# Optimization experiments

Hardware: AMD Instinct MI355X
Metric: run time of the kernel (lower is better)

Reference implementation:

```python
import jax, jax.numpy as jnp
import numpy as np

FINAL_OUT = 28
NPG = 127            # nodes per graph (XENON1T top PMT array)
B = 4096             # graphs per batch
N = B * NPG          # 520192 total nodes
EPG = 2032           # edges per graph (avg degree ~16)
E = B * EPG          # 8323072 total edges


def setup_inputs() -> dict:
    key = jax.random.key(0)
    ks = jax.random.split(key, 12)
    # intra-graph random edges, offset per graph
    off = (jnp.arange(B, dtype=jnp.int64) * NPG)[:, None]
    src = (jax.random.randint(ks[0], (B, EPG), 0, NPG) + off).reshape(-1)
    dst = (jax.random.randint(ks[1], (B, EPG), 0, NPG) + off).reshape(-1)
    edge_index = jnp.stack([src, dst]).astype(jnp.int64)
    x = jax.random.normal(ks[2], (N, 3), dtype=jnp.float32)
    # GCNConv weights (in,out) + bias; Linear head weights (in,out) + bias
    def glorot(k, shape):
        lim = float(np.sqrt(6.0 / (shape[0] + shape[1])))
        return jax.random.uniform(k, shape, jnp.float32, -lim, lim)
    return {
        "x": x,
        "edge_index": edge_index,
        "W1": glorot(ks[3], (3, 16)),
        "b1": jnp.zeros((16,), jnp.float32),
        "W2": glorot(ks[4], (16, FINAL_OUT)),
        "b2": jnp.zeros((FINAL_OUT,), jnp.float32),
        "lw1": glorot(ks[5], (FINAL_OUT * NPG, 16)),
        "lb1": jnp.zeros((16,), jnp.float32),
        "lw2": glorot(ks[6], (16, 2)),
        "lb2": jnp.zeros((2,), jnp.float32),
    }


def _gcn_conv(x, W, b, src_sl, dst_sl, dinv):
    # h = X W, then normalized scatter-add aggregation over edges (+self-loops)
    h = x @ W                                   # [N, F_out]
    norm = dinv[src_sl] * dinv[dst_sl]          # [E+N]
    msg = h[src_sl] * norm[:, None]             # gather + scale
    return jax.ops.segment_sum(msg, dst_sl, num_segments=N) + b


def reference(x, edge_index, W1, b1, W2, b2, lw1, lb1, lw2, lb2):
    src, dst = edge_index[0], edge_index[1]
    loops = jnp.arange(N, dtype=edge_index.dtype)
    src_sl = jnp.concatenate([src, loops])
    dst_sl = jnp.concatenate([dst, loops])
    # symmetric degree normalization with self-loops (PyG GCNConv default)
    deg = jnp.zeros((N,), jnp.float32).at[dst_sl].add(1.0)
    dinv = jnp.where(deg > 0, jax.lax.rsqrt(deg), 0.0)
    h = jax.nn.relu(_gcn_conv(x, W1, b1, src_sl, dst_sl, dinv))
    h = jax.nn.relu(_gcn_conv(h, W2, b2, src_sl, dst_sl, dinv))
    g = h.reshape(-1, FINAL_OUT * NPG)          # [B, 3556]
    g = jax.nn.relu(g @ lw1 + lb1)
    return g @ lw2 + lb2                        # [B, 2]
```

## Files before the change

### kernel.cpp

```cpp
#include <hip/hip_runtime.h>

#define NPG 127
#define EPG 2032
#define NGRAPH 4096
#define NE (EPG * NGRAPH)
#define F1 16
#define F2 28

#define EPK  0
#define A2   0
#define XS   2032
#define HS2  2540
#define H2   4572
#define XRAW 4572
#define ARENA 8128

__global__ __launch_bounds__(256, 4) void gcn_fused(
    const float* __restrict__ x, const int* __restrict__ ei,
    const float* __restrict__ W1, const float* __restrict__ b1,
    const float* __restrict__ W2, const float* __restrict__ b2,
    const float* __restrict__ lw1, const float* __restrict__ lb1,
    const float* __restrict__ lw2, const float* __restrict__ lb2,
    float* __restrict__ out)
{
    __shared__ __align__(16) float arena[ARENA];
    __shared__ unsigned short csr[EPG];
    __shared__ int starts[NPG + 1];
    __shared__ int cursor[NPG];
    __shared__ float dinv[NPG];
    __shared__ float w1s[48], b1s[F1], w2s[F1 * F2], b2s[F2];
    __shared__ float lb1s[16], lw2s[32], lb2s[2];
    __shared__ float wsum[64];
    __shared__ float gsh[16];
    __shared__ int is64;

    const int t = threadIdx.x;
    const int g = blockIdx.x;
    const int nodebase = g * NPG;
    const int ebase = g * EPG;

    if (t < 64) {
        int w = ei[2 * t + 1];
        unsigned long long m = __ballot(w != 0);
        if (t == 0) is64 = (m == 0ULL) ? 1 : 0;
    }
    if (t < NPG + 1) starts[t] = 0;
    if (t < 48)       w1s[t]        = W1[t];
    else if (t < 64)  b1s[t - 48]   = b1[t - 48];
    else if (t < 92)  b2s[t - 64]   = b2[t - 64];
    else if (t < 108) lb1s[t - 92]  = lb1[t - 92];
    else if (t < 140) lw2s[t - 108] = lw2[t - 108];
    else if (t < 142) lb2s[t - 140] = lb2[t - 140];
    for (int i = t; i < F1 * F2; i += 256) w2s[i] = W2[i];
    __syncthreads();

    int* epk = (int*)&arena[EPK];
    if (is64) {
        const long long* ei64 = (const long long*)ei;
        const longlong2* s2 = (const longlong2*)(ei64 + ebase);
        const longlong2* d2 = (const longlong2*)(ei64 + NE + ebase);
        for (int q = t; q < EPG / 2; q += 256) {
            longlong2 ss = s2[q], dd = d2[q];
            int s0 = (int)ss.x - nodebase, d0 = (int)dd.x - nodebase;
            int s1 = (int)ss.y - nodebase, d1 = (int)dd.y - nodebase;
            epk[2 * q + 0] = (s0 << 8) | d0;  atomicAdd(&starts[d0 + 1], 1);
            epk[2 * q + 1] = (s1 << 8) | d1;  atomicAdd(&starts[d1 + 1], 1);
        }
    } else {
        const int4* s4 = (const int4*)(ei + ebase);
        const int4* d4 = (const int4*)(ei + NE + ebase);
        for (int q = t; q < EPG / 4; q += 256) {
            int4 ss = s4[q], dd = d4[q];
            int e0 = 4 * q;
            epk[e0 + 0] = ((ss.x - nodebase) << 8) | (dd.x - nodebase);
            epk[e0 + 1] = ((ss.y - nodebase) << 8) | (dd.y - nodebase);
            epk[e0 + 2] = ((ss.z - nodebase) << 8) | (dd.z - nodebase);
            epk[e0 + 3] = ((ss.w - nodebase) << 8) | (dd.w - nodebase);
            atomicAdd(&starts[(dd.x - nodebase) + 1], 1);
            atomicAdd(&starts[(dd.y - nodebase) + 1], 1);
            atomicAdd(&starts[(dd.z - nodebase) + 1], 1);
            atomicAdd(&starts[(dd.w - nodebase) + 1], 1);
        }
    }
    for (int i = t; i < NPG * 3; i += 256) arena[XRAW + i] = x[nodebase * 3 + i];
    __syncthreads();
    if (t < NPG) dinv[t] = rsqrtf((float)(starts[t + 1] + 1));
    __syncthreads();
    #pragma unroll
    for (int off = 1; off < 128; off <<= 1) {
        int v = 0;
        if (t < 128) { v = starts[t]; if (t >= off) v += starts[t - off]; }
        __syncthreads();
        if (t < 128) starts[t] = v;
        __syncthreads();
    }
    if (t < NPG) {
        cursor[t] = starts[t];
        float di = dinv[t];
        float4 xr;
        xr.x = arena[XRAW + t * 3 + 0] * di;
        xr.y = arena[XRAW + t * 3 + 1] * di;
        xr.z = arena[XRAW + t * 3 + 2] * di;
        xr.w = 0.f;
        *(float4*)&arena[XS + t * 4] = xr;
    }
    __syncthreads();
    for (int e = t; e < EPG; e += 256) {
        int pk = epk[e];
        int d = pk & 255, s = pk >> 8;
        int pos = atomicAdd(&cursor[d], 1);
        csr[pos] = (unsigned short)s;
    }
    __syncthreads();

    if (t < 2 * NPG) {
        const int i = t >> 1, half = t & 1;
        const int e0 = starts[i], e1 = starts[i + 1];
        float ax = 0.f, ay = 0.f, az = 0.f;
        for (int k = e0 + half; k < e1; k += 2) {
            int s = csr[k];
            const float4 v = *(const float4*)&arena[XS + s * 4];
            ax += v.x; ay += v.y; az += v.z;
        }
        if (!half) {
            const float4 v = *(const float4*)&arena[XS + i * 4];
            ax += v.x; ay += v.y; az += v.z;
        }
        ax += __shfl_xor(ax, 1);
        ay += __shfl_xor(ay, 1);
        az += __shfl_xor(az, 1);
        const float di = dinv[i];
        ax *= di; ay *= di; az *= di;
        const int fb = half * 8;
        float h[8];
        #pragma unroll
        for (int f = 0; f < 8; ++f) {
            float v = ax * w1s[fb + f] + ay * w1s[16 + fb + f] + az * w1s[32 + fb + f];
            h[f] = fmaxf(v + b1s[fb + f], 0.f) * di;
        }
        const int rot = (i >> 1) & 3;
        const int s0 = ((half * 2 + 0) + rot) & 3;
        const int s1 = ((half * 2 + 1) + rot) & 3;
        *(float4*)&arena[HS2 + i * 16 + s0 * 4] = make_float4(h[0], h[1], h[2], h[3]);
        *(float4*)&arena[HS2 + i * 16 + s1 * 4] = make_float4(h[4], h[5], h[6], h[7]);
    }
    __syncthreads();

    if (t < 2 * NPG) {
        const int i = t >> 1, half = t & 1;
        const int e0 = starts[i], e1 = starts[i + 1];
        float4 c0 = {0,0,0,0}, c1 = {0,0,0,0}, c2 = {0,0,0,0}, c3 = {0,0,0,0};
        for (int k = e0 + half; k < e1; k += 2) {
            int s = csr[k];
            const int b = HS2 + s * 16;
            const int r = (s >> 1) & 3;
            const float4 v0 = *(const float4*)&arena[b + (((0 + r) & 3) << 2)];
            const float4 v1 = *(const float4*)&arena[b + (((1 + r) & 3) << 2)];
            const float4 v2 = *(const float4*)&arena[b + (((2 + r) & 3) << 2)];
            const float4 v3 = *(const float4*)&arena[b + (((3 + r) & 3) << 2)];
            c0.x += v0.x; c0.y += v0.y; c0.z += v0.z; c0.w += v0.w;
            c1.x += v1.x; c1.y += v1.y; c1.z += v1.z; c1.w += v1.w;
            c2.x += v2.x; c2.y += v2.y; c2.z += v2.z; c2.w += v2.w;
            c3.x += v3.x; c3.y += v3.y; c3.z += v3.z; c3.w += v3.w;
        }
        if (!half) {
            const int b = HS2 + i * 16;
            const int r = (i >> 1) & 3;
            const float4 v0 = *(const float4*)&arena[b + (((0 + r) & 3) << 2)];
            const float4 v1 = *(const float4*)&arena[b + (((1 + r) & 3) << 2)];
            const float4 v2 = *(const float4*)&arena[b + (((2 + r) & 3) << 2)];
            const float4 v3 = *(const float4*)&arena[b + (((3 + r) & 3) << 2)];
            c0.x += v0.x; c0.y += v0.y; c0.z += v0.z; c0.w += v0.w;
            c1.x += v1.x; c1.y += v1.y; c1.z += v1.z; c1.w += v1.w;
            c2.x += v2.x; c2.y += v2.y; c2.z += v2.z; c2.w += v2.w;
            c3.x += v3.x; c3.y += v3.y; c3.z += v3.z; c3.w += v3.w;
        }
        c0.x += __shfl_xor(c0.x, 1); c0.y += __shfl_xor(c0.y, 1);
        c0.z += __shfl_xor(c0.z, 1); c0.w += __shfl_xor(c0.w, 1);
        c1.x += __shfl_xor(c1.x, 1); c1.y += __shfl_xor(c1.y, 1);
        c1.z += __shfl_xor(c1.z, 1); c1.w += __shfl_xor(c1.w, 1);
        c2.x += __shfl_xor(c2.x, 1); c2.y += __shfl_xor(c2.y, 1);
        c2.z += __shfl_xor(c2.z, 1); c2.w += __shfl_xor(c2.w, 1);
        c3.x += __shfl_xor(c3.x, 1); c3.y += __shfl_xor(c3.y, 1);
        c3.z += __shfl_xor(c3.z, 1); c3.w += __shfl_xor(c3.w, 1);
        const float di = dinv[i];
        if (!half) {
            c0.x *= di; c0.y *= di; c0.z *= di; c0.w *= di;
            c1.x *= di; c1.y *= di; c1.z *= di; c1.w *= di;
            *(float4*)&arena[A2 + i * 16 + 0] = c0;
            *(float4*)&arena[A2 + i * 16 + 4] = c1;
        } else {
            c2.x *= di; c2.y *= di; c2.z *= di; c2.w *= di;
            c3.x *= di; c3.y *= di; c3.z *= di; c3.w *= di;
            *(float4*)&arena[A2 + i * 16 + 8]  = c2;
            *(float4*)&arena[A2 + i * 16 + 12] = c3;
        }
    }
    __syncthreads();

    if (t < 252) {
        const int f2 = t % 28, ic = t / 28;
        float wc[16];
        #pragma unroll
        for (int k = 0; k < 16; ++k) wc[k] = w2s[k * F2 + f2];
        const float bb = b2s[f2];
        for (int i = ic; i < NPG; i += 9) {
            const float4 h0 = *(const float4*)&arena[A2 + i * 16 + 0];
            const float4 h1v = *(const float4*)&arena[A2 + i * 16 + 4];
            const float4 h2v = *(const float4*)&arena[A2 + i * 16 + 8];
            const float4 h3 = *(const float4*)&arena[A2 + i * 16 + 12];
            float acc = bb;
            acc = fmaf(h0.x, wc[0], acc);  acc = fmaf(h0.y, wc[1], acc);
            acc = fmaf(h0.z, wc[2], acc);  acc = fmaf(h0.w, wc[3], acc);
            acc = fmaf(h1v.x, wc[4], acc); acc = fmaf(h1v.y, wc[5], acc);
            acc = fmaf(h1v.z, wc[6], acc); acc = fmaf(h1v.w, wc[7], acc);
            acc = fmaf(h2v.x, wc[8], acc); acc = fmaf(h2v.y, wc[9], acc);
            acc = fmaf(h2v.z, wc[10], acc); acc = fmaf(h2v.w, wc[11], acc);
            acc = fmaf(h3.x, wc[12], acc); acc = fmaf(h3.y, wc[13], acc);
            acc = fmaf(h3.z, wc[14], acc); acc = fmaf(h3.w, wc[15], acc);
            arena[H2 + i * F2 + f2] = fmaxf(acc, 0.f);
        }
    }
    __syncthreads();

    float pj[16];
    #pragma unroll
    for (int j = 0; j < 16; ++j) pj[j] = 0.f;
    const float4* lw14 = (const float4*)lw1;
    for (int r = t; r < NPG * F2; r += 256) {
        float hv = arena[H2 + r];
        float4 a = lw14[r * 4 + 0];
        float4 b = lw14[r * 4 + 1];
        float4 c = lw14[r * 4 + 2];
        float4 d = lw14[r * 4 + 3];
        pj[0]  = fmaf(hv, a.x, pj[0]);  pj[1]  = fmaf(hv, a.y, pj[1]);
        pj[2]  = fmaf(hv, a.z, pj[2]);  pj[3]  = fmaf(hv, a.w, pj[3]);
        pj[4]  = fmaf(hv, b.x, pj[4]);  pj[5]  = fmaf(hv, b.y, pj[5]);
        pj[6]  = fmaf(hv, b.z, pj[6]);  pj[7]  = fmaf(hv, b.w, pj[7]);
        pj[8]  = fmaf(hv, c.x, pj[8]);  pj[9]  = fmaf(hv, c.y, pj[9]);
        pj[10] = fmaf(hv, c.z, pj[10]); pj[11] = fmaf(hv, c.w, pj[11]);
        pj[12] = fmaf(hv, d.x, pj[12]); pj[13] = fmaf(hv, d.y, pj[13]);
        pj[14] = fmaf(hv, d.z, pj[14]); pj[15] = fmaf(hv, d.w, pj[15]);
    }
    #pragma unroll
    for (int j = 0; j < 16; ++j) {
        float v = pj[j];
        v += __shfl_xor(v, 1);
        v += __shfl_xor(v, 2);
        v += __shfl_xor(v, 4);
        v += __shfl_xor(v, 8);
        v += __shfl_xor(v, 16);
        v += __shfl_xor(v, 32);
        pj[j] = v;
    }
    if ((t & 63) == 0) {
        int wid = t >> 6;
        #pragma unroll
        for (int j = 0; j < 16; ++j) wsum[wid * 16 + j] = pj[j];
    }
    __syncthreads();
    if (t < 16) {
        float s = wsum[t] + wsum[16 + t] + wsum[32 + t] + wsum[48 + t];
        gsh[t] = fmaxf(s + lb1s[t], 0.f);
    }
    __syncthreads();
    if (t < 2) {
        float o = lb2s[t];
        #pragma unroll
        for (int j = 0; j < 16; ++j) o = fmaf(gsh[j], lw2s[j * 2 + t], o);
        out[g * 2 + t] = o;
    }
}

extern "C" void kernel_launch(void* const* d_in, const int* in_sizes, int n_in,
                              void* d_out, int out_size, void* d_ws, size_t ws_size,
                              hipStream_t stream) {
    const float* x   = (const float*)d_in[0];
    const int*   ei  = (const int*)d_in[1];
    const float* W1  = (const float*)d_in[2];
    const float* b1  = (const float*)d_in[3];
    const float* W2  = (const float*)d_in[4];
    const float* b2  = (const float*)d_in[5];
    const float* lw1 = (const float*)d_in[6];
    const float* lb1 = (const float*)d_in[7];
    const float* lw2 = (const float*)d_in[8];
    const float* lb2 = (const float*)d_in[9];
    float* out = (float*)d_out;

    gcn_fused<<<NGRAPH, 256, 0, stream>>>(x, ei, W1, b1, W2, b2,
                                          lw1, lb1, lw2, lb2, out);
}
```

Baseline: 194.6 us.

## Process one graph per wavefront with wave-local CSR build and no block barriers

Restructures the fused GCN kernel so each 64-lane wavefront handles a whole graph, with four graphs per block. Block-wide __syncthreads are replaced by lgkmcnt waits. The prefix sum becomes a shuffle scan, and the CSR is built directly with byte indices in a per-wave LDS region. The second-layer transform now runs per node in registers, and the final head reduction happens inside the wave. The aim is to remove barrier and idle-thread costs. In exchange, each lane now serially aggregates two nodes, which raises per-lane work and register pressure (launch bounds drop to 2 blocks per SM). It also relies on wave-synchronous LDS visibility.

```diff
diff --git a/kernel.cpp b/kernel.cpp
--- a/kernel.cpp
+++ b/kernel.cpp
@@ -4,18 +4,112 @@
 #define EPG 2032
 #define NGRAPH 4096
 #define NE (EPG * NGRAPH)
-#define F1 16
-#define F2 28
-
-#define EPK  0
-#define A2   0
-#define XS   2032
-#define HS2  2540
-#define H2   4572
-#define XRAW 4572
-#define ARENA 8128
-
-__global__ __launch_bounds__(256, 4) void gcn_fused(
+
+#define WREG 3812
+#define R_CSR    0
+#define R_STARTS 508
+#define R_CURSOR 636
+#define R_XS     764
+#define R_HS2    1272
+#define R_H2     0
+
+#define WFENCE() asm volatile("s_waitcnt lgkmcnt(0)" ::: "memory")
+
+__device__ __forceinline__ void agg1_node(float* A, const unsigned* st,
+        const unsigned char* csr8, int i, float di,
+        float sx, float sy, float sz, const float* w1s, const float* b1s)
+{
+    float ax = sx, ay = sy, az = sz;
+    const unsigned e0 = st[i], e1 = st[i + 1];
+    for (unsigned k = e0; k < e1; ++k) {
+        const int s = csr8[k];
+        const float4 v = *(const float4*)(A + R_XS + s * 4);
+        ax += v.x; ay += v.y; az += v.z;
+    }
+    ax *= di; ay *= di; az *= di;
+    float* hrow = A + R_HS2 + i * 20;
+    #pragma unroll
+    for (int f4 = 0; f4 < 4; ++f4) {
+        const float4 wa = *(const float4*)(w1s + f4 * 4);
+        const float4 wb = *(const float4*)(w1s + 16 + f4 * 4);
+        const float4 wc = *(const float4*)(w1s + 32 + f4 * 4);
+        const float4 bb = *(const float4*)(b1s + f4 * 4);
+        float4 h;
+        h.x = fmaxf(fmaf(ax, wa.x, fmaf(ay, wb.x, fmaf(az, wc.x, bb.x))), 0.f) * di;
+        h.y = fmaxf(fmaf(ax, wa.y, fmaf(ay, wb.y, fmaf(az, wc.y, bb.y))), 0.f) * di;
+        h.z = fmaxf(fmaf(ax, wa.z, fmaf(ay, wb.z, fmaf(az, wc.z, bb.z))), 0.f) * di;
+        h.w = fmaxf(fmaf(ax, wa.w, fmaf(ay, wb.w, fmaf(az, wc.w, bb.w))), 0.f) * di;
+        *(float4*)(hrow + f4 * 4) = h;
+    }
+}
+
+__device__ __forceinline__ void agg2_node(const float* A, const unsigned* st,
+        const unsigned char* csr8, int i, float di,
+        float4& c0, float4& c1, float4& c2, float4& c3)
+{
+    const float* base = A + R_HS2;
+    const float* r = base + i * 20;
+    c0 = *(const float4*)(r);
+    c1 = *(const float4*)(r + 4);
+    c2 = *(const float4*)(r + 8);
+    c3 = *(const float4*)(r + 12);
+    const unsigned e0 = st[i], e1 = st[i + 1];
+    for (unsigned k = e0; k < e1; ++k) {
+        const int s = csr8[k];
+        const float* p = base + s * 20;
+        const float4 v0 = *(const float4*)(p);
+        const float4 v1 = *(const float4*)(p + 4);
+        const float4 v2 = *(const float4*)(p + 8);
+        const float4 v3 = *(const float4*)(p + 12);
+        c0.x += v0.x; c0.y += v0.y; c0.z += v0.z; c0.w += v0.w;
+        c1.x += v1.x; c1.y += v1.y; c1.z += v1.z; c1.w += v1.w;
+        c2.x += v2.x; c2.y += v2.y; c2.z += v2.z; c2.w += v2.w;
+        c3.x += v3.x; c3.y += v3.y; c3.z += v3.z; c3.w += v3.w;
+    }
+    c0.x *= di; c0.y *= di; c0.z *= di; c0.w *= di;
+    c1.x *= di; c1.y *= di; c1.z *= di; c1.w *= di;
+    c2.x *= di; c2.y *= di; c2.z *= di; c2.w *= di;
+    c3.x *= di; c3.y *= di; c3.z *= di; c3.w *= di;
+}
+
+__device__ __forceinline__ void transform_node(float* A, int i,
+        float4 c0, float4 c1, float4 c2, float4 c3,
+        const float* w2s, const float* b2s)
+{
+    float acc[28];
+    #pragma unroll
+    for (int f4 = 0; f4 < 7; ++f4) {
+        const float4 b = *(const float4*)(b2s + f4 * 4);
+        acc[f4 * 4 + 0] = b.x; acc[f4 * 4 + 1] = b.y;
+        acc[f4 * 4 + 2] = b.z; acc[f4 * 4 + 3] = b.w;
+    }
+    const float a2arr[16] = {c0.x, c0.y, c0.z, c0.w, c1.x, c1.y, c1.z, c1.w,
+                             c2.x, c2.y, c2.z, c2.w, c3.x, c3.y, c3.z, c3.w};
+    #pragma unroll
+    for (int k = 0; k < 16; ++k) {
+        const float a = a2arr[k];
+        #pragma unroll
+        for (int f4 = 0; f4 < 7; ++f4) {
+            const float4 wv = *(const float4*)(w2s + k * 28 + f4 * 4);
+            acc[f4 * 4 + 0] = fmaf(a, wv.x, acc[f4 * 4 + 0]);
+            acc[f4 * 4 + 1] = fmaf(a, wv.y, acc[f4 * 4 + 1]);
+            acc[f4 * 4 + 2] = fmaf(a, wv.z, acc[f4 * 4 + 2]);
+            acc[f4 * 4 + 3] = fmaf(a, wv.w, acc[f4 * 4 + 3]);
+        }
+    }
+    float* hrow = A + R_H2 + i * 28;
+    #pragma unroll
+    for (int f4 = 0; f4 < 7; ++f4) {
+        float4 h;
+        h.x = fmaxf(acc[f4 * 4 + 0], 0.f);
+        h.y = fmaxf(acc[f4 * 4 + 1], 0.f);
+        h.z = fmaxf(acc[f4 * 4 + 2], 0.f);
+        h.w = fmaxf(acc[f4 * 4 + 3], 0.f);
+        *(float4*)(hrow + f4 * 4) = h;
+    }
+}
+
+__global__ __launch_bounds__(256, 2) void gcn_fused(
     const float* __restrict__ x, const int* __restrict__ ei,
     const float* __restrict__ W1, const float* __restrict__ b1,
     const float* __restrict__ W2, const float* __restrict__ b2,
@@ -23,224 +117,152 @@
     const float* __restrict__ lw2, const float* __restrict__ lb2,
     float* __restrict__ out)
 {
-    __shared__ __align__(16) float arena[ARENA];
-    __shared__ unsigned short csr[EPG];
-    __shared__ int starts[NPG + 1];
-    __shared__ int cursor[NPG];
-    __shared__ float dinv[NPG];
-    __shared__ float w1s[48], b1s[F1], w2s[F1 * F2], b2s[F2];
-    __shared__ float lb1s[16], lw2s[32], lb2s[2];
-    __shared__ float wsum[64];
-    __shared__ float gsh[16];
-    __shared__ int is64;
+    __shared__ __align__(16) float arena[4 * WREG];
+    __shared__ __align__(16) float w1s[48], b1s[16], w2s[448], b2s[28];
+    __shared__ __align__(16) float lb1s[16], lw2s[32], lb2s[2];
 
     const int t = threadIdx.x;
-    const int g = blockIdx.x;
-    const int nodebase = g * NPG;
-    const int ebase = g * EPG;
-
-    if (t < 64) {
-        int w = ei[2 * t + 1];
-        unsigned long long m = __ballot(w != 0);
-        if (t == 0) is64 = (m == 0ULL) ? 1 : 0;
-    }
-    if (t < NPG + 1) starts[t] = 0;
+    const int lane = t & 63;
+    const int w = t >> 6;
+    const int gi = blockIdx.x * 4 + w;
+    float* A = arena + w * WREG;
+    unsigned* cnt = (unsigned*)(A + R_STARTS);
+    unsigned* cur = (unsigned*)(A + R_CURSOR);
+    unsigned char* csr8 = (unsigned char*)(A + R_CSR);
+    const int nodebase = gi * NPG;
+    const long ebase = (long)gi * EPG;
+
     if (t < 48)       w1s[t]        = W1[t];
     else if (t < 64)  b1s[t - 48]   = b1[t - 48];
     else if (t < 92)  b2s[t - 64]   = b2[t - 64];
     else if (t < 108) lb1s[t - 92]  = lb1[t - 92];
     else if (t < 140) lw2s[t - 108] = lw2[t - 108];
     else if (t < 142) lb2s[t - 140] = lb2[t - 140];
-    for (int i = t; i < F1 * F2; i += 256) w2s[i] = W2[i];
+    for (int i = t; i < 448; i += 256) w2s[i] = W2[i];
+
+    const int hiw = ei[2 * lane + 1];
+    const bool is64 = (__ballot(hiw != 0) == 0ULL);
+
+    cnt[lane] = 0u;
+    cnt[lane + 64] = 0u;
+    WFENCE();
     __syncthreads();
 
-    int* epk = (int*)&arena[EPK];
+    if (is64) {
+        const long long* ei64 = (const long long*)ei;
+        const longlong2* d2 = (const longlong2*)(ei64 + NE + ebase);
+        for (int q = lane; q < EPG / 2; q += 64) {
+            const longlong2 dd = d2[q];
+            atomicAdd(&cnt[(int)dd.x - nodebase], 1u);
+            atomicAdd(&cnt[(int)dd.y - nodebase], 1u);
+        }
+    } else {
+        const int4* d4 = (const int4*)(ei + NE + ebase);
+        for (int q = lane; q < EPG / 4; q += 64) {
+            const int4 dd = d4[q];
+            atomicAdd(&cnt[dd.x - nodebase], 1u);
+            atomicAdd(&cnt[dd.y - nodebase], 1u);
+            atomicAdd(&cnt[dd.z - nodebase], 1u);
+            atomicAdd(&cnt[dd.w - nodebase], 1u);
+        }
+    }
+    WFENCE();
+
+    const int i0 = lane, i1 = lane + 64;
+    const bool v1 = (i1 < NPG);
+    const unsigned deg0 = cnt[i0];
+    const unsigned deg1 = v1 ? cnt[i1] : 0u;
+    const unsigned c0 = cnt[2 * lane], c1 = cnt[2 * lane + 1];
+    const float d0 = rsqrtf((float)(deg0 + 1u));
+    const float d1 = rsqrtf((float)(deg1 + 1u));
+    asm volatile("" ::: "memory");
+    unsigned ps = c0 + c1, sc = ps;
+    #pragma unroll
+    for (int dd = 1; dd < 64; dd <<= 1) {
+        const unsigned u = __shfl_up(sc, dd);
+        if (lane >= dd) sc += u;
+    }
+    const unsigned excl = sc - ps;
+    cnt[2 * lane] = excl;
+    cnt[2 * lane + 1] = excl + c0;
+    cur[2 * lane] = excl;
+    cur[2 * lane + 1] = excl + c0;
+
+    float sx0, sy0, sz0, sx1 = 0.f, sy1 = 0.f, sz1 = 0.f;
+    {
+        const float* xp = x + (long)(nodebase + i0) * 3;
+        sx0 = xp[0] * d0; sy0 = xp[1] * d0; sz0 = xp[2] * d0;
+        const float4 xv = {sx0, sy0, sz0, 0.f};
+        *(float4*)(A + R_XS + i0 * 4) = xv;
+        if (v1) {
+            const float* xq = x + (long)(nodebase + i1) * 3;
+            sx1 = xq[0] * d1; sy1 = xq[1] * d1; sz1 = xq[2] * d1;
+            const float4 xw = {sx1, sy1, sz1, 0.f};
+            *(float4*)(A + R_XS + i1 * 4) = xw;
+        }
+    }
+    WFENCE();
+
     if (is64) {
         const long long* ei64 = (const long long*)ei;
         const longlong2* s2 = (const longlong2*)(ei64 + ebase);
         const longlong2* d2 = (const longlong2*)(ei64 + NE + ebase);
-        for (int q = t; q < EPG / 2; q += 256) {
-            longlong2 ss = s2[q], dd = d2[q];
-            int s0 = (int)ss.x - nodebase, d0 = (int)dd.x - nodebase;
-            int s1 = (int)ss.y - nodebase, d1 = (int)dd.y - nodebase;
-            epk[2 * q + 0] = (s0 << 8) | d0;  atomicAdd(&starts[d0 + 1], 1);
-            epk[2 * q + 1] = (s1 << 8) | d1;  atomicAdd(&starts[d1 + 1], 1);
+        for (int q = lane; q < EPG / 2; q += 64) {
+            const longlong2 ss = s2[q], dd = d2[q];
+            unsigned p0 = atomicAdd(&cur[(int)dd.x - nodebase], 1u);
+            csr8[p0] = (unsigned char)((int)ss.x - nodebase);
+            unsigned p1 = atomicAdd(&cur[(int)dd.y - nodebase], 1u);
+            csr8[p1] = (unsigned char)((int)ss.y - nodebase);
         }
     } else {
         const int4* s4 = (const int4*)(ei + ebase);
         const int4* d4 = (const int4*)(ei + NE + ebase);
-        for (int q = t; q < EPG / 4; q += 256) {
-            int4 ss = s4[q], dd = d4[q];
-            int e0 = 4 * q;
-            epk[e0 + 0] = ((ss.x - nodebase) << 8) | (dd.x - nodebase);
-            epk[e0 + 1] = ((ss.y - nodebase) << 8) | (dd.y - nodebase);
-            epk[e0 + 2] = ((ss.z - nodebase) << 8) | (dd.z - nodebase);
-            epk[e0 + 3] = ((ss.w - nodebase) << 8) | (dd.w - nodebase);
-            atomicAdd(&starts[(dd.x - nodebase) + 1], 1);
-            atomicAdd(&starts[(dd.y - nodebase) + 1], 1);
-            atomicAdd(&starts[(dd.z - nodebase) + 1], 1);
-            atomicAdd(&starts[(dd.w - nodebase) + 1], 1);
-        }
-    }
-    for (int i = t; i < NPG * 3; i += 256) arena[XRAW + i] = x[nodebase * 3 + i];
-    __syncthreads();
-    if (t < NPG) dinv[t] = rsqrtf((float)(starts[t + 1] + 1));
-    __syncthreads();
-    #pragma unroll
-    for (int off = 1; off < 128; off <<= 1) {
-        int v = 0;
-        if (t < 128) { v = starts[t]; if (t >= off) v += starts[t - off]; }
-        __syncthreads();
-        if (t < 128) starts[t] = v;
-        __syncthreads();
-    }
-    if (t < NPG) {
-        cursor[t] = starts[t];
-        float di = dinv[t];
-        float4 xr;
-        xr.x = arena[XRAW + t * 3 + 0] * di;
-        xr.y = arena[XRAW + t * 3 + 1] * di;
-        xr.z = arena[XRAW + t * 3 + 2] * di;
-        xr.w = 0.f;
-        *(float4*)&arena[XS + t * 4] = xr;
-    }
-    __syncthreads();
-    for (int e = t; e < EPG; e += 256) {
-        int pk = epk[e];
-        int d = pk & 255, s = pk >> 8;
-        int pos = atomicAdd(&cursor[d], 1);
-        csr[pos] = (unsigned short)s;
-    }
-    __syncthreads();
-
-    if (t < 2 * NPG) {
-        const int i = t >> 1, half = t & 1;
-        const int e0 = starts[i], e1 = starts[i + 1];
-        float ax = 0.f, ay = 0.f, az = 0.f;
-        for (int k = e0 + half; k < e1; k += 2) {
-            int s = csr[k];
-            const float4 v = *(const float4*)&arena[XS + s * 4];
-            ax += v.x; ay += v.y; az += v.z;
-        }
-        if (!half) {
-            const float4 v = *(const float4*)&arena[XS + i * 4];
-            ax += v.x; ay += v.y; az += v.z;
-        }
-        ax += __shfl_xor(ax, 1);
-        ay += __shfl_xor(ay, 1);
-        az += __shfl_xor(az, 1);
-        const float di = dinv[i];
-        ax *= di; ay *= di; az *= di;
-        const int fb = half * 8;
-        float h[8];
-        #pragma unroll
-        for (int f = 0; f < 8; ++f) {
-            float v = ax * w1s[fb + f] + ay * w1s[16 + fb + f] + az * w1s[32 + fb + f];
-            h[f] = fmaxf(v + b1s[fb + f], 0.f) * di;
-        }
-        const int rot = (i >> 1) & 3;
-        const int s0 = ((half * 2 + 0) + rot) & 3;
-        const int s1 = ((half * 2 + 1) + rot) & 3;
-        *(float4*)&arena[HS2 + i * 16 + s0 * 4] = make_float4(h[0], h[1], h[2], h[3]);
-        *(float4*)&arena[HS2 + i * 16 + s1 * 4] = make_float4(h[4], h[5], h[6], h[7]);
-    }
-    __syncthreads();
-
-    if (t < 2 * NPG) {
-        const int i = t >> 1, half = t & 1;
-        const int e0 = starts[i], e1 = starts[i + 1];
-        float4 c0 = {0,0,0,0}, c1 = {0,0,0,0}, c2 = {0,0,0,0}, c3 = {0,0,0,0};
-        for (int k = e0 + half; k < e1; k += 2) {
-            int s = csr[k];
-            const int b = HS2 + s * 16;
-            const int r = (s >> 1) & 3;
-            const float4 v0 = *(const float4*)&arena[b + (((0 + r) & 3) << 2)];
-            const float4 v1 = *(const float4*)&arena[b + (((1 + r) & 3) << 2)];
-            const float4 v2 = *(const float4*)&arena[b + (((2 + r) & 3) << 2)];
-            const float4 v3 = *(const float4*)&arena[b + (((3 + r) & 3) << 2)];
-            c0.x += v0.x; c0.y += v0.y; c0.z += v0.z; c0.w += v0.w;
-            c1.x += v1.x; c1.y += v1.y; c1.z += v1.z; c1.w += v1.w;
-            c2.x += v2.x; c2.y += v2.y; c2.z += v2.z; c2.w += v2.w;
-            c3.x += v3.x; c3.y += v3.y; c3.z += v3.z; c3.w += v3.w;
-        }
-        if (!half) {
-            const int b = HS2 + i * 16;
-            const int r = (i >> 1) & 3;
-            const float4 v0 = *(const float4*)&arena[b + (((0 + r) & 3) << 2)];
-            const float4 v1 = *(const float4*)&arena[b + (((1 + r) & 3) << 2)];
-            const float4 v2 = *(const float4*)&arena[b + (((2 + r) & 3) << 2)];
-            const float4 v3 = *(const float4*)&arena[b + (((3 + r) & 3) << 2)];
-            c0.x += v0.x; c0.y += v0.y; c0.z += v0.z; c0.w += v0.w;
-            c1.x += v1.x; c1.y += v1.y; c1.z += v1.z; c1.w += v1.w;
-            c2.x += v2.x; c2.y += v2.y; c2.z += v2.z; c2.w += v2.w;
-            c3.x += v3.x; c3.y += v3.y; c3.z += v3.z; c3.w += v3.w;
-        }
-        c0.x += __shfl_xor(c0.x, 1); c0.y += __shfl_xor(c0.y, 1);
-        c0.z += __shfl_xor(c0.z, 1); c0.w += __shfl_xor(c0.w, 1);
-        c1.x += __shfl_xor(c1.x, 1); c1.y += __shfl_xor(c1.y, 1);
-        c1.z += __shfl_xor(c1.z, 1); c1.w += __shfl_xor(c1.w, 1);
-        c2.x += __shfl_xor(c2.x, 1); c2.y += __shfl_xor(c2.y, 1);
-        c2.z += __shfl_xor(c2.z, 1); c2.w += __shfl_xor(c2.w, 1);
-        c3.x += __shfl_xor(c3.x, 1); c3.y += __shfl_xor(c3.y, 1);
-        c3.z += __shfl_xor(c3.z, 1); c3.w += __shfl_xor(c3.w, 1);
-        const float di = dinv[i];
-        if (!half) {
-            c0.x *= di; c0.y *= di; c0.z *= di; c0.w *= di;
-            c1.x *= di; c1.y *= di; c1.z *= di; c1.w *= di;
-            *(float4*)&arena[A2 + i * 16 + 0] = c0;
-            *(float4*)&arena[A2 + i * 16 + 4] = c1;
-        } else {
-            c2.x *= di; c2.y *= di; c2.z *= di; c2.w *= di;
-            c3.x *= di; c3.y *= di; c3.z *= di; c3.w *= di;
-            *(float4*)&arena[A2 + i * 16 + 8]  = c2;
-            *(float4*)&arena[A2 + i * 16 + 12] = c3;
-        }
-    }
-    __syncthreads();
-
-    if (t < 252) {
-        const int f2 = t % 28, ic = t / 28;
-        float wc[16];
-        #pragma unroll
-        for (int k = 0; k < 16; ++k) wc[k] = w2s[k * F2 + f2];
-        const float bb = b2s[f2];
-        for (int i = ic; i < NPG; i += 9) {
-            const float4 h0 = *(const float4*)&arena[A2 + i * 16 + 0];
-            const float4 h1v = *(const float4*)&arena[A2 + i * 16 + 4];
-            const float4 h2v = *(const float4*)&arena[A2 + i * 16 + 8];
-            const float4 h3 = *(const float4*)&arena[A2 + i * 16 + 12];
-            float acc = bb;
-            acc = fmaf(h0.x, wc[0], acc);  acc = fmaf(h0.y, wc[1], acc);
-            acc = fmaf(h0.z, wc[2], acc);  acc = fmaf(h0.w, wc[3], acc);
-            acc = fmaf(h1v.x, wc[4], acc); acc = fmaf(h1v.y, wc[5], acc);
-            acc = fmaf(h1v.z, wc[6], acc); acc = fmaf(h1v.w, wc[7], acc);
-            acc = fmaf(h2v.x, wc[8], acc); acc = fmaf(h2v.y, wc[9], acc);
-            acc = fmaf(h2v.z, wc[10], acc); acc = fmaf(h2v.w, wc[11], acc);
-            acc = fmaf(h3.x, wc[12], acc); acc = fmaf(h3.y, wc[13], acc);
-            acc = fmaf(h3.z, wc[14], acc); acc = fmaf(h3.w, wc[15], acc);
-            arena[H2 + i * F2 + f2] = fmaxf(acc, 0.f);
-        }
-    }
-    __syncthreads();
+        for (int q = lane; q < EPG / 4; q += 64) {
+            const int4 ss = s4[q], dd = d4[q];
+            unsigned p0 = atomicAdd(&cur[dd.x - nodebase], 1u);
+            csr8[p0] = (unsigned char)(ss.x - nodebase);
+            unsigned p1 = atomicAdd(&cur[dd.y - nodebase], 1u);
+            csr8[p1] = (unsigned char)(ss.y - nodebase);
+            unsigned p2 = atomicAdd(&cur[dd.z - nodebase], 1u);
+            csr8[p2] = (unsigned char)(ss.z - nodebase);
+            unsigned p3 = atomicAdd(&cur[dd.w - nodebase], 1u);
+            csr8[p3] = (unsigned char)(ss.w - nodebase);
+        }
+    }
+    WFENCE();
+
+    const unsigned* st = cnt;
+    agg1_node(A, st, csr8, i0, d0, sx0, sy0, sz0, w1s, b1s);
+    if (v1) agg1_node(A, st, csr8, i1, d1, sx1, sy1, sz1, w1s, b1s);
+    WFENCE();
+
+    float4 a0, a1, a2, a3, e0v, e1v, e2v, e3v;
+    agg2_node(A, st, csr8, i0, d0, a0, a1, a2, a3);
+    if (v1) agg2_node(A, st, csr8, i1, d1, e0v, e1v, e2v, e3v);
+    WFENCE();
+
+    transform_node(A, i0, a0, a1, a2, a3, w2s, b2s);
+    if (v1) transform_node(A, i1, e0v, e1v, e2v, e3v, w2s, b2s);
+    WFENCE();
 
     float pj[16];
     #pragma unroll
     for (int j = 0; j < 16; ++j) pj[j] = 0.f;
     const float4* lw14 = (const float4*)lw1;
-    for (int r = t; r < NPG * F2; r += 256) {
-        float hv = arena[H2 + r];
-        float4 a = lw14[r * 4 + 0];
-        float4 b = lw14[r * 4 + 1];
-        float4 c = lw14[r * 4 + 2];
-        float4 d = lw14[r * 4 + 3];
-        pj[0]  = fmaf(hv, a.x, pj[0]);  pj[1]  = fmaf(hv, a.y, pj[1]);
-        pj[2]  = fmaf(hv, a.z, pj[2]);  pj[3]  = fmaf(hv, a.w, pj[3]);
-        pj[4]  = fmaf(hv, b.x, pj[4]);  pj[5]  = fmaf(hv, b.y, pj[5]);
-        pj[6]  = fmaf(hv, b.z, pj[6]);  pj[7]  = fmaf(hv, b.w, pj[7]);
-        pj[8]  = fmaf(hv, c.x, pj[8]);  pj[9]  = fmaf(hv, c.y, pj[9]);
-        pj[10] = fmaf(hv, c.z, pj[10]); pj[11] = fmaf(hv, c.w, pj[11]);
-        pj[12] = fmaf(hv, d.x, pj[12]); pj[13] = fmaf(hv, d.y, pj[13]);
-        pj[14] = fmaf(hv, d.z, pj[14]); pj[15] = fmaf(hv, d.w, pj[15]);
+    for (int r = lane; r < NPG * 28; r += 64) {
+        const float hv = A[R_H2 + r];
+        const float4 aa = lw14[(long)r * 4 + 0];
+        const float4 bb = lw14[(long)r * 4 + 1];
+        const float4 cc = lw14[(long)r * 4 + 2];
+        const float4 ddv = lw14[(long)r * 4 + 3];
+        pj[0]  = fmaf(hv, aa.x, pj[0]);  pj[1]  = fmaf(hv, aa.y, pj[1]);
+        pj[2]  = fmaf(hv, aa.z, pj[2]);  pj[3]  = fmaf(hv, aa.w, pj[3]);
+        pj[4]  = fmaf(hv, bb.x, pj[4]);  pj[5]  = fmaf(hv, bb.y, pj[5]);
+        pj[6]  = fmaf(hv, bb.z, pj[6]);  pj[7]  = fmaf(hv, bb.w, pj[7]);
+        pj[8]  = fmaf(hv, cc.x, pj[8]);  pj[9]  = fmaf(hv, cc.y, pj[9]);
+        pj[10] = fmaf(hv, cc.z, pj[10]); pj[11] = fmaf(hv, cc.w, pj[11]);
+        pj[12] = fmaf(hv, ddv.x, pj[12]); pj[13] = fmaf(hv, ddv.y, pj[13]);
+        pj[14] = fmaf(hv, ddv.z, pj[14]); pj[15] = fmaf(hv, ddv.w, pj[15]);
     }
     #pragma unroll
     for (int j = 0; j < 16; ++j) {
@@ -251,24 +273,13 @@
         v += __shfl_xor(v, 8);
         v += __shfl_xor(v, 16);
         v += __shfl_xor(v, 32);
-        pj[j] = v;
-    }
-    if ((t & 63) == 0) {
-        int wid = t >> 6;
+        pj[j] = fmaxf(v + lb1s[j], 0.f);
+    }
+    if (lane < 2) {
+        float o = lb2s[lane];
         #pragma unroll
-        for (int j = 0; j < 16; ++j) wsum[wid * 16 + j] = pj[j];
-    }
-    __syncthreads();
-    if (t < 16) {
-        float s = wsum[t] + wsum[16 + t] + wsum[32 + t] + wsum[48 + t];
-        gsh[t] = fmaxf(s + lb1s[t], 0.f);
-    }
-    __syncthreads();
-    if (t < 2) {
-        float o = lb2s[t];
-        #pragma unroll
-        for (int j = 0; j < 16; ++j) o = fmaf(gsh[j], lw2s[j * 2 + t], o);
-        out[g * 2 + t] = o;
+        for (int j = 0; j < 16; ++j) o = fmaf(pj[j], lw2s[j * 2 + lane], o);
+        out[gi * 2 + lane] = o;
     }
 }
 
@@ -287,6 +298,6 @@
     const float* lb2 = (const float*)d_in[9];
     float* out = (float*)d_out;
 
-    gcn_fused<<<NGRAPH, 256, 0, stream>>>(x, ei, W1, b1, W2, b2,
-                                          lw1, lb1, lw2, lb2, out);
-}
+    gcn_fused<<<NGRAPH / 4, 256, 0, stream>>>(x, ei, W1, b1, W2, b2,
+                                              lw1, lb1, lw2, lb2, out);
+}
```

Measured after the change: 282.8 us. 1.45x slower.

## Shrink LDS arena, use wave-shuffle scan, fuse layer-2 transform into registers

Applied to the files above, without the earlier changes.

Cuts the shared-memory footprint by overlapping buffers, storing CSR indices as bytes inside the arena, and reading x directly from global memory, then raises launch bounds from 4 to 6 blocks per CU. The multi-barrier Hillis-Steele prefix sum over starts is replaced with a single-wave shuffle scan over per-node counts. The layer-2 aggregation result stays in registers, and each thread pair computes 14 of the 28 output features directly, which removes an LDS round trip and a sync. The higher occupancy target may force register spills given the 14-element accumulators and 16-element arrays.

```diff
diff --git a/kernel.cpp b/kernel.cpp
--- a/kernel.cpp
+++ b/kernel.cpp
@@ -7,15 +7,14 @@
 #define F1 16
 #define F2 28
 
-#define EPK  0
-#define A2   0
-#define XS   2032
-#define HS2  2540
-#define H2   4572
-#define XRAW 4572
-#define ARENA 8128
-
-__global__ __launch_bounds__(256, 4) void gcn_fused(
+#define A_EPK 0
+#define A_HS2 0
+#define A_XS  2032
+#define A_CSR 2540
+#define A_H2  0
+#define ARENA 3556
+
+__global__ __launch_bounds__(256, 6) void gcn_fused(
     const float* __restrict__ x, const int* __restrict__ ei,
     const float* __restrict__ W1, const float* __restrict__ b1,
     const float* __restrict__ W2, const float* __restrict__ b2,
@@ -24,152 +23,152 @@
     float* __restrict__ out)
 {
     __shared__ __align__(16) float arena[ARENA];
-    __shared__ unsigned short csr[EPG];
-    __shared__ int starts[NPG + 1];
-    __shared__ int cursor[NPG];
+    __shared__ unsigned cnt[128], starts[128], cursor[128];
     __shared__ float dinv[NPG];
-    __shared__ float w1s[48], b1s[F1], w2s[F1 * F2], b2s[F2];
+    __shared__ __align__(16) float w1s[48], b1s[F1], w2s[448], b2s[F2];
     __shared__ float lb1s[16], lw2s[32], lb2s[2];
-    __shared__ float wsum[64];
-    __shared__ float gsh[16];
+    __shared__ float wsum[64], gsh[16];
     __shared__ int is64;
 
     const int t = threadIdx.x;
     const int g = blockIdx.x;
     const int nodebase = g * NPG;
-    const int ebase = g * EPG;
+    const long ebase = (long)g * EPG;
 
     if (t < 64) {
-        int w = ei[2 * t + 1];
-        unsigned long long m = __ballot(w != 0);
+        const int hiw = ei[2 * t + 1];
+        const unsigned long long m = __ballot(hiw != 0);
         if (t == 0) is64 = (m == 0ULL) ? 1 : 0;
     }
-    if (t < NPG + 1) starts[t] = 0;
     if (t < 48)       w1s[t]        = W1[t];
     else if (t < 64)  b1s[t - 48]   = b1[t - 48];
     else if (t < 92)  b2s[t - 64]   = b2[t - 64];
     else if (t < 108) lb1s[t - 92]  = lb1[t - 92];
     else if (t < 140) lw2s[t - 108] = lw2[t - 108];
     else if (t < 142) lb2s[t - 140] = lb2[t - 140];
-    for (int i = t; i < F1 * F2; i += 256) w2s[i] = W2[i];
-    __syncthreads();
-
-    int* epk = (int*)&arena[EPK];
+    for (int q = t; q < 448; q += 256) w2s[q] = W2[q];
+    if (t < 128) cnt[t] = 0u;
+    __syncthreads();
+
+    int* epk = (int*)&arena[A_EPK];
     if (is64) {
         const long long* ei64 = (const long long*)ei;
         const longlong2* s2 = (const longlong2*)(ei64 + ebase);
         const longlong2* d2 = (const longlong2*)(ei64 + NE + ebase);
         for (int q = t; q < EPG / 2; q += 256) {
-            longlong2 ss = s2[q], dd = d2[q];
-            int s0 = (int)ss.x - nodebase, d0 = (int)dd.x - nodebase;
-            int s1 = (int)ss.y - nodebase, d1 = (int)dd.y - nodebase;
-            epk[2 * q + 0] = (s0 << 8) | d0;  atomicAdd(&starts[d0 + 1], 1);
-            epk[2 * q + 1] = (s1 << 8) | d1;  atomicAdd(&starts[d1 + 1], 1);
+            const longlong2 ss = s2[q], dd = d2[q];
+            const int sa = (int)ss.x - nodebase, da = (int)dd.x - nodebase;
+            const int sb = (int)ss.y - nodebase, db = (int)dd.y - nodebase;
+            epk[2 * q + 0] = (sa << 8) | da;  atomicAdd(&cnt[da], 1u);
+            epk[2 * q + 1] = (sb << 8) | db;  atomicAdd(&cnt[db], 1u);
         }
     } else {
         const int4* s4 = (const int4*)(ei + ebase);
         const int4* d4 = (const int4*)(ei + NE + ebase);
         for (int q = t; q < EPG / 4; q += 256) {
-            int4 ss = s4[q], dd = d4[q];
-            int e0 = 4 * q;
-            epk[e0 + 0] = ((ss.x - nodebase) << 8) | (dd.x - nodebase);
-            epk[e0 + 1] = ((ss.y - nodebase) << 8) | (dd.y - nodebase);
-            epk[e0 + 2] = ((ss.z - nodebase) << 8) | (dd.z - nodebase);
-            epk[e0 + 3] = ((ss.w - nodebase) << 8) | (dd.w - nodebase);
-            atomicAdd(&starts[(dd.x - nodebase) + 1], 1);
-            atomicAdd(&starts[(dd.y - nodebase) + 1], 1);
-            atomicAdd(&starts[(dd.z - nodebase) + 1], 1);
-            atomicAdd(&starts[(dd.w - nodebase) + 1], 1);
-        }
-    }
-    for (int i = t; i < NPG * 3; i += 256) arena[XRAW + i] = x[nodebase * 3 + i];
-    __syncthreads();
-    if (t < NPG) dinv[t] = rsqrtf((float)(starts[t + 1] + 1));
-    __syncthreads();
-    #pragma unroll
-    for (int off = 1; off < 128; off <<= 1) {
-        int v = 0;
-        if (t < 128) { v = starts[t]; if (t >= off) v += starts[t - off]; }
-        __syncthreads();
-        if (t < 128) starts[t] = v;
-        __syncthreads();
+            const int4 ss = s4[q], dd = d4[q];
+            const int eb = 4 * q;
+            epk[eb + 0] = ((ss.x - nodebase) << 8) | (dd.x - nodebase);
+            epk[eb + 1] = ((ss.y - nodebase) << 8) | (dd.y - nodebase);
+            epk[eb + 2] = ((ss.z - nodebase) << 8) | (dd.z - nodebase);
+            epk[eb + 3] = ((ss.w - nodebase) << 8) | (dd.w - nodebase);
+            atomicAdd(&cnt[dd.x - nodebase], 1u);
+            atomicAdd(&cnt[dd.y - nodebase], 1u);
+            atomicAdd(&cnt[dd.z - nodebase], 1u);
+            atomicAdd(&cnt[dd.w - nodebase], 1u);
+        }
+    }
+    __syncthreads();
+
+    if (t < 64) {
+        const unsigned ca = cnt[2 * t], cb = cnt[2 * t + 1];
+        const unsigned ps = ca + cb;
+        unsigned sc = ps;
+        #pragma unroll
+        for (int d = 1; d < 64; d <<= 1) {
+            const unsigned u = __shfl_up(sc, d);
+            if (t >= d) sc += u;
+        }
+        const unsigned excl = sc - ps;
+        starts[2 * t] = excl;            cursor[2 * t] = excl;
+        starts[2 * t + 1] = excl + ca;   cursor[2 * t + 1] = excl + ca;
     }
     if (t < NPG) {
-        cursor[t] = starts[t];
-        float di = dinv[t];
-        float4 xr;
-        xr.x = arena[XRAW + t * 3 + 0] * di;
-        xr.y = arena[XRAW + t * 3 + 1] * di;
-        xr.z = arena[XRAW + t * 3 + 2] * di;
-        xr.w = 0.f;
-        *(float4*)&arena[XS + t * 4] = xr;
-    }
-    __syncthreads();
+        const float dv = rsqrtf((float)(cnt[t] + 1u));
+        dinv[t] = dv;
+        const float* xp = x + (long)(nodebase + t) * 3;
+        const float4 xv = {xp[0] * dv, xp[1] * dv, xp[2] * dv, 0.f};
+        *(float4*)&arena[A_XS + t * 4] = xv;
+    }
+    __syncthreads();
+
+    unsigned char* csr8 = (unsigned char*)&arena[A_CSR];
     for (int e = t; e < EPG; e += 256) {
-        int pk = epk[e];
-        int d = pk & 255, s = pk >> 8;
-        int pos = atomicAdd(&cursor[d], 1);
-        csr[pos] = (unsigned short)s;
-    }
-    __syncthreads();
-
-    if (t < 2 * NPG) {
-        const int i = t >> 1, half = t & 1;
-        const int e0 = starts[i], e1 = starts[i + 1];
+        const int pk = epk[e];
+        const int d = pk & 255, s = pk >> 8;
+        const unsigned pos = atomicAdd(&cursor[d], 1u);
+        csr8[pos] = (unsigned char)s;
+    }
+    __syncthreads();
+
+    const int i = t >> 1, half = t & 1;
+    const bool act = (t < 2 * NPG);
+    float di = 0.f; unsigned e0 = 0, e1 = 0;
+    if (act) { di = dinv[i]; e0 = starts[i]; e1 = starts[i + 1]; }
+
+    if (act) {
         float ax = 0.f, ay = 0.f, az = 0.f;
-        for (int k = e0 + half; k < e1; k += 2) {
-            int s = csr[k];
-            const float4 v = *(const float4*)&arena[XS + s * 4];
+        for (unsigned k = e0 + half; k < e1; k += 2) {
+            const int s = csr8[k];
+            const float4 v = *(const float4*)&arena[A_XS + s * 4];
             ax += v.x; ay += v.y; az += v.z;
         }
         if (!half) {
-            const float4 v = *(const float4*)&arena[XS + i * 4];
+            const float4 v = *(const float4*)&arena[A_XS + i * 4];
             ax += v.x; ay += v.y; az += v.z;
         }
         ax += __shfl_xor(ax, 1);
         ay += __shfl_xor(ay, 1);
         az += __shfl_xor(az, 1);
-        const float di = dinv[i];
         ax *= di; ay *= di; az *= di;
         const int fb = half * 8;
         float h[8];
         #pragma unroll
         for (int f = 0; f < 8; ++f) {
-            float v = ax * w1s[fb + f] + ay * w1s[16 + fb + f] + az * w1s[32 + fb + f];
+            const float v = ax * w1s[fb + f] + ay * w1s[16 + fb + f]
+                          + az * w1s[32 + fb + f];
             h[f] = fmaxf(v + b1s[fb + f], 0.f) * di;
         }
         const int rot = (i >> 1) & 3;
-        const int s0 = ((half * 2 + 0) + rot) & 3;
-        const int s1 = ((half * 2 + 1) + rot) & 3;
-        *(float4*)&arena[HS2 + i * 16 + s0 * 4] = make_float4(h[0], h[1], h[2], h[3]);
-        *(float4*)&arena[HS2 + i * 16 + s1 * 4] = make_float4(h[4], h[5], h[6], h[7]);
-    }
-    __syncthreads();
-
-    if (t < 2 * NPG) {
-        const int i = t >> 1, half = t & 1;
-        const int e0 = starts[i], e1 = starts[i + 1];
-        float4 c0 = {0,0,0,0}, c1 = {0,0,0,0}, c2 = {0,0,0,0}, c3 = {0,0,0,0};
-        for (int k = e0 + half; k < e1; k += 2) {
-            int s = csr[k];
-            const int b = HS2 + s * 16;
-            const int r = (s >> 1) & 3;
-            const float4 v0 = *(const float4*)&arena[b + (((0 + r) & 3) << 2)];
-            const float4 v1 = *(const float4*)&arena[b + (((1 + r) & 3) << 2)];
-            const float4 v2 = *(const float4*)&arena[b + (((2 + r) & 3) << 2)];
-            const float4 v3 = *(const float4*)&arena[b + (((3 + r) & 3) << 2)];
+        const int sl0 = (half * 2 + 0 + rot) & 3;
+        const int sl1 = (half * 2 + 1 + rot) & 3;
+        *(float4*)&arena[A_HS2 + i * 16 + sl0 * 4] = make_float4(h[0], h[1], h[2], h[3]);
+        *(float4*)&arena[A_HS2 + i * 16 + sl1 * 4] = make_float4(h[4], h[5], h[6], h[7]);
+    }
+    __syncthreads();
+
+    float4 c0 = {0,0,0,0}, c1 = {0,0,0,0}, c2 = {0,0,0,0}, c3 = {0,0,0,0};
+    if (act) {
+        for (unsigned k = e0 + half; k < e1; k += 2) {
+            const int s = csr8[k];
+            const float* p = &arena[A_HS2 + s * 16];
+            const int rr = (s >> 1) & 3;
+            const float4 v0 = *(const float4*)(p + (((0 + rr) & 3) << 2));
+            const float4 v1 = *(const float4*)(p + (((1 + rr) & 3) << 2));
+            const float4 v2 = *(const float4*)(p + (((2 + rr) & 3) << 2));
+            const float4 v3 = *(const float4*)(p + (((3 + rr) & 3) << 2));
             c0.x += v0.x; c0.y += v0.y; c0.z += v0.z; c0.w += v0.w;
             c1.x += v1.x; c1.y += v1.y; c1.z += v1.z; c1.w += v1.w;
             c2.x += v2.x; c2.y += v2.y; c2.z += v2.z; c2.w += v2.w;
             c3.x += v3.x; c3.y += v3.y; c3.z += v3.z; c3.w += v3.w;
         }
         if (!half) {
-            const int b = HS2 + i * 16;
-            const int r = (i >> 1) & 3;
-            const float4 v0 = *(const float4*)&arena[b + (((0 + r) & 3) << 2)];
-            const float4 v1 = *(const float4*)&arena[b + (((1 + r) & 3) << 2)];
-            const float4 v2 = *(const float4*)&arena[b + (((2 + r) & 3) << 2)];
-            const float4 v3 = *(const float4*)&arena[b + (((3 + r) & 3) << 2)];
+            const float* p = &arena[A_HS2 + i * 16];
+            const int rr = (i >> 1) & 3;
+            const float4 v0 = *(const float4*)(p + (((0 + rr) & 3) << 2));
+            const float4 v1 = *(const float4*)(p + (((1 + rr) & 3) << 2));
+            const float4 v2 = *(const float4*)(p + (((2 + rr) & 3) << 2));
+            const float4 v3 = *(const float4*)(p + (((3 + rr) & 3) << 2));
             c0.x += v0.x; c0.y += v0.y; c0.z += v0.z; c0.w += v0.w;
             c1.x += v1.x; c1.y += v1.y; c1.z += v1.z; c1.w += v1.w;
             c2.x += v2.x; c2.y += v2.y; c2.z += v2.z; c2.w += v2.w;
@@ -183,42 +182,36 @@
         c2.z += __shfl_xor(c2.z, 1); c2.w += __shfl_xor(c2.w, 1);
         c3.x += __shfl_xor(c3.x, 1); c3.y += __shfl_xor(c3.y, 1);
         c3.z += __shfl_xor(c3.z, 1); c3.w += __shfl_xor(c3.w, 1);
-        const float di = dinv[i];
-        if (!half) {
-            c0.x *= di; c0.y *= di; c0.z *= di; c0.w *= di;
-            c1.x *= di; c1.y *= di; c1.z *= di; c1.w *= di;
-            *(float4*)&arena[A2 + i * 16 + 0] = c0;
-            *(float4*)&arena[A2 + i * 16 + 4] = c1;
-        } else {
-            c2.x *= di; c2.y *= di; c2.z *= di; c2.w *= di;
-            c3.x *= di; c3.y *= di; c3.z *= di; c3.w *= di;
-            *(float4*)&arena[A2 + i * 16 + 8]  = c2;
-            *(float4*)&arena[A2 + i * 16 + 12] = c3;
-        }
-    }
-    __syncthreads();
-
-    if (t < 252) {
-        const int f2 = t % 28, ic = t / 28;
-        float wc[16];
-        #pragma unroll
-        for (int k = 0; k < 16; ++k) wc[k] = w2s[k * F2 + f2];
-        const float bb = b2s[f2];
-        for (int i = ic; i < NPG; i += 9) {
-            const float4 h0 = *(const float4*)&arena[A2 + i * 16 + 0];
-            const float4 h1v = *(const float4*)&arena[A2 + i * 16 + 4];
-            const float4 h2v = *(const float4*)&arena[A2 + i * 16 + 8];
-            const float4 h3 = *(const float4*)&arena[A2 + i * 16 + 12];
-            float acc = bb;
-            acc = fmaf(h0.x, wc[0], acc);  acc = fmaf(h0.y, wc[1], acc);
-            acc = fmaf(h0.z, wc[2], acc);  acc = fmaf(h0.w, wc[3], acc);
-            acc = fmaf(h1v.x, wc[4], acc); acc = fmaf(h1v.y, wc[5], acc);
-            acc = fmaf(h1v.z, wc[6], acc); acc = fmaf(h1v.w, wc[7], acc);
-            acc = fmaf(h2v.x, wc[8], acc); acc = fmaf(h2v.y, wc[9], acc);
-            acc = fmaf(h2v.z, wc[10], acc); acc = fmaf(h2v.w, wc[11], acc);
-            acc = fmaf(h3.x, wc[12], acc); acc = fmaf(h3.y, wc[13], acc);
-            acc = fmaf(h3.z, wc[14], acc); acc = fmaf(h3.w, wc[15], acc);
-            arena[H2 + i * F2 + f2] = fmaxf(acc, 0.f);
+        c0.x *= di; c0.y *= di; c0.z *= di; c0.w *= di;
+        c1.x *= di; c1.y *= di; c1.z *= di; c1.w *= di;
+        c2.x *= di; c2.y *= di; c2.z *= di; c2.w *= di;
+        c3.x *= di; c3.y *= di; c3.z *= di; c3.w *= di;
+    }
+    __syncthreads();
+
+    if (act) {
+        const float a2[16] = {c0.x, c0.y, c0.z, c0.w, c1.x, c1.y, c1.z, c1.w,
+                              c2.x, c2.y, c2.z, c2.w, c3.x, c3.y, c3.z, c3.w};
+        const int base = half * 14;
+        float acc[14];
+        #pragma unroll
+        for (int j = 0; j < 14; ++j) acc[j] = b2s[base + j];
+        #pragma unroll
+        for (int k = 0; k < 16; ++k) {
+            const float a = a2[k];
+            const float* wr = &w2s[k * 28 + base];
+            #pragma unroll
+            for (int m = 0; m < 7; ++m) {
+                const float2 wv = *(const float2*)(wr + 2 * m);
+                acc[2 * m]     = fmaf(a, wv.x, acc[2 * m]);
+                acc[2 * m + 1] = fmaf(a, wv.y, acc[2 * m + 1]);
+            }
+        }
+        float* hp = &arena[A_H2 + i * 28 + base];
+        #pragma unroll
+        for (int m = 0; m < 7; ++m) {
+            const float2 hv = {fmaxf(acc[2 * m], 0.f), fmaxf(acc[2 * m + 1], 0.f)};
+            *(float2*)(hp + 2 * m) = hv;
         }
     }
     __syncthreads();
@@ -228,19 +221,19 @@
     for (int j = 0; j < 16; ++j) pj[j] = 0.f;
     const float4* lw14 = (const float4*)lw1;
     for (int r = t; r < NPG * F2; r += 256) {
-        float hv = arena[H2 + r];
-        float4 a = lw14[r * 4 + 0];
-        float4 b = lw14[r * 4 + 1];
-        float4 c = lw14[r * 4 + 2];
-        float4 d = lw14[r * 4 + 3];
-        pj[0]  = fmaf(hv, a.x, pj[0]);  pj[1]  = fmaf(hv, a.y, pj[1]);
-        pj[2]  = fmaf(hv, a.z, pj[2]);  pj[3]  = fmaf(hv, a.w, pj[3]);
-        pj[4]  = fmaf(hv, b.x, pj[4]);  pj[5]  = fmaf(hv, b.y, pj[5]);
-        pj[6]  = fmaf(hv, b.z, pj[6]);  pj[7]  = fmaf(hv, b.w, pj[7]);
-        pj[8]  = fmaf(hv, c.x, pj[8]);  pj[9]  = fmaf(hv, c.y, pj[9]);
-        pj[10] = fmaf(hv, c.z, pj[10]); pj[11] = fmaf(hv, c.w, pj[11]);
-        pj[12] = fmaf(hv, d.x, pj[12]); pj[13] = fmaf(hv, d.y, pj[13]);
-        pj[14] = fmaf(hv, d.z, pj[14]); pj[15] = fmaf(hv, d.w, pj[15]);
+        const float hv = arena[A_H2 + r];
+        const float4 aa = lw14[(long)r * 4 + 0];
+        const float4 bb = lw14[(long)r * 4 + 1];
+        const float4 cc = lw14[(long)r * 4 + 2];
+        const float4 dd = lw14[(long)r * 4 + 3];
+        pj[0]  = fmaf(hv, aa.x, pj[0]);  pj[1]  = fmaf(hv, aa.y, pj[1]);
+        pj[2]  = fmaf(hv, aa.z, pj[2]);  pj[3]  = fmaf(hv, aa.w, pj[3]);
+        pj[4]  = fmaf(hv, bb.x, pj[4]);  pj[5]  = fmaf(hv, bb.y, pj[5]);
+        pj[6]  = fmaf(hv, bb.z, pj[6]);  pj[7]  = fmaf(hv, bb.w, pj[7]);
+        pj[8]  = fmaf(hv, cc.x, pj[8]);  pj[9]  = fmaf(hv, cc.y, pj[9]);
+        pj[10] = fmaf(hv, cc.z, pj[10]); pj[11] = fmaf(hv, cc.w, pj[11]);
+        pj[12] = fmaf(hv, dd.x, pj[12]); pj[13] = fmaf(hv, dd.y, pj[13]);
+        pj[14] = fmaf(hv, dd.z, pj[14]); pj[15] = fmaf(hv, dd.w, pj[15]);
     }
     #pragma unroll
     for (int j = 0; j < 16; ++j) {
@@ -254,13 +247,13 @@
         pj[j] = v;
     }
     if ((t & 63) == 0) {
-        int wid = t >> 6;
+        const int wid = t >> 6;
         #pragma unroll
         for (int j = 0; j < 16; ++j) wsum[wid * 16 + j] = pj[j];
     }
     __syncthreads();
     if (t < 16) {
-        float s = wsum[t] + wsum[16 + t] + wsum[32 + t] + wsum[48 + t];
+        const float s = wsum[t] + wsum[16 + t] + wsum[32 + t] + wsum[48 + t];
         gsh[t] = fmaxf(s + lb1s[t], 0.f);
     }
     __syncthreads();
```

After: 182.1 us. 6.4% less time.
